# Kernel tuning notes

Hardware: AMD Instinct MI355X
Metric: run time of the kernel (lower is better)

The kernel has to match this reference:

```python
import jax, jax.numpy as jnp
import numpy as np

H = 256   # input_size
P = 256   # state_size
BATCH, L = 8, 4096
DT_MIN, DT_MAX = 1e-3, 1e-1
LN_EPS = 1e-5


def _hippo_params():
    # HiPPO-N matrix (num_blocks=1), eigendecomposition in numpy (float64 then cast)
    idx = np.arange(P, dtype=np.float64)
    s = np.sqrt(idx + 0.5)
    A = -np.outer(s, s)
    A = np.tril(A) - np.triu(A, 1)
    np.fill_diagonal(A, -0.5)
    ev, V = np.linalg.eig(A)
    order = np.argsort(ev.real)
    ev, V = ev[order], V[:, order]
    return ev, V


def setup_inputs() -> dict:
    key = jax.random.key(0)
    k_u, = jax.random.split(key, 1)
    ev, V = _hippo_params()
    rng = np.random.default_rng(0)
    log_lambda_real = np.log(-np.clip(ev.real, None, -1e-4)).astype(np.float32)
    lambda_imag = ev.imag.astype(np.float32)
    V_inv = np.linalg.inv(V)
    B_init = rng.standard_normal((P, H)) / np.sqrt(P)
    B_tilde = V_inv @ B_init.astype(np.complex128)
    C_init = rng.standard_normal((H, P)) / np.sqrt(P)
    C_tilde = C_init.astype(np.complex128) @ V
    log_delta = (rng.random(P) * (np.log(DT_MAX) - np.log(DT_MIN)) + np.log(DT_MIN)).astype(np.float32)
    return {
        "u": jax.random.normal(k_u, (BATCH, L, H), dtype=jnp.float32),
        "log_lambda_real": jnp.asarray(log_lambda_real),
        "lambda_imag": jnp.asarray(lambda_imag),
        "B_tilde_real": jnp.asarray(B_tilde.real, dtype=jnp.float32),
        "B_tilde_imag": jnp.asarray(B_tilde.imag, dtype=jnp.float32),
        "C_tilde_real": jnp.asarray(C_tilde.real, dtype=jnp.float32),
        "C_tilde_imag": jnp.asarray(C_tilde.imag, dtype=jnp.float32),
        "log_delta": jnp.asarray(log_delta),
        "gamma": jnp.ones((H,), dtype=jnp.float32),
        "beta": jnp.zeros((H,), dtype=jnp.float32),
    }


def _layernorm(x, gamma, beta):
    mu = jnp.mean(x, axis=-1, keepdims=True)
    var = jnp.mean(jnp.square(x - mu), axis=-1, keepdims=True)
    return (x - mu) * jax.lax.rsqrt(var + LN_EPS) * gamma + beta


def _ssm(h, log_lambda_real, lambda_imag, B_tilde_real, B_tilde_imag,
         C_tilde_real, C_tilde_imag, log_delta):
    # Continuous-time diagonal SSM params
    lam = -jnp.exp(log_lambda_real) + 1j * lambda_imag            # (P,) complex
    B_tilde = B_tilde_real + 1j * B_tilde_imag                     # (P,H)
    C_tilde = C_tilde_real + 1j * C_tilde_imag                     # (H,P)
    delta = jnp.exp(log_delta)                                     # (P,)
    # ZOH discretization (eq. 6 of the S5 paper)
    lambda_bar = jnp.exp(lam * delta)                              # (P,)
    B_bar = ((lambda_bar - 1.0) / lam)[:, None] * B_tilde          # (P,H)
    # Bu_k = B_bar @ u_k  ->  (B,L,P) complex
    Bu = jnp.einsum('blh,ph->blp', h.astype(jnp.complex64), B_bar.astype(jnp.complex64))
    # Parallel associative scan for x_k = lambda_bar * x_{k-1} + Bu_k
    a = jnp.broadcast_to(lambda_bar.astype(jnp.complex64), Bu.shape)
    def combine(c1, c2):
        a1, b1 = c1
        a2, b2 = c2
        return a1 * a2, a2 * b1 + b2
    _, xs = jax.lax.associative_scan(combine, (a, Bu), axis=1)     # (B,L,P)
    # Project back to real output: y = Re(C_tilde @ x)
    y = jnp.einsum('blp,hp->blh', xs, C_tilde.astype(jnp.complex64)).real
    return y


def reference(u, log_lambda_real, lambda_imag, B_tilde_real, B_tilde_imag,
              C_tilde_real, C_tilde_imag, log_delta, gamma, beta):
    # S5Block: pre-LayerNorm -> S5 SSM -> GELU -> residual
    h = _layernorm(u, gamma, beta)
    y = _ssm(h, log_lambda_real, lambda_imag, B_tilde_real, B_tilde_imag,
             C_tilde_real, C_tilde_imag, log_delta)
    return u + jax.nn.gelu(y)
```

## Files before the change

### kernel.cpp

```cpp
#include <hip/hip_runtime.h>
#include <math.h>

#define HDIM 256
#define PDIM 256
#define BATCH 8
#define LSEQ 4096
#define MTOT (BATCH * LSEQ)
#define NCHUNK 128
#define CHLEN 32

typedef __attribute__((ext_vector_type(8))) short bf16x8;
typedef __attribute__((ext_vector_type(4))) float f32x4;

__device__ __forceinline__ unsigned short f2bf(float f) {
    union { float f; unsigned int u; } v; v.f = f;
    unsigned int r = v.u + 0x7FFFu + ((v.u >> 16) & 1u);
    return (unsigned short)(r >> 16);
}
__device__ __forceinline__ float bf2f(unsigned int lo16) {
    union { unsigned int u; float f; } v; v.u = lo16 << 16;
    return v.f;
}

__global__ void params_k(const float* __restrict__ llr, const float* __restrict__ lim,
                         const float* __restrict__ ldl, float* __restrict__ par) {
    int p = threadIdx.x;
    float er = expf(llr[p]);
    float im = lim[p];
    float d  = expf(ldl[p]);
    float zr = -er * d, zi = im * d;
    float ea = expf(zr);
    float ar = ea * cosf(zi), ai = ea * sinf(zi);
    float dr = -er, di = im;
    float den = dr * dr + di * di;
    float nr = ar - 1.0f, ni = ai;
    float cr = (nr * dr + ni * di) / den;
    float ci = (ni * dr - nr * di) / den;
    float eC = expf((float)CHLEN * zr);
    float sC, cC;
    sincosf((float)CHLEN * zi, &sC, &cC);
    par[2 * p]           = ar;
    par[2 * p + 1]       = ai;
    par[512 + 2 * p]     = cr;
    par[512 + 2 * p + 1] = ci;
    par[1024 + 2 * p]     = eC * cC;
    par[1024 + 2 * p + 1] = eC * sC;
}

__global__ void w1_k(const float* __restrict__ Br, const float* __restrict__ Bi,
                     const float* __restrict__ par, unsigned short* __restrict__ W1t) {
    int p = blockIdx.x, h = threadIdx.x;
    float cr = par[512 + 2 * p], ci = par[512 + 2 * p + 1];
    float br = Br[p * HDIM + h], bi = Bi[p * HDIM + h];
    W1t[(2 * p) * HDIM + h]     = f2bf(cr * br - ci * bi);
    W1t[(2 * p + 1) * HDIM + h] = f2bf(cr * bi + ci * br);
}

__global__ void w2_k(const float* __restrict__ Cr, const float* __restrict__ Ci,
                     unsigned short* __restrict__ W2t) {
    int p = blockIdx.x, h = threadIdx.x;
    W2t[h * (2 * PDIM) + 2 * p]     = f2bf(Cr[h * PDIM + p]);
    W2t[h * (2 * PDIM) + 2 * p + 1] = f2bf(-Ci[h * PDIM + p]);
}

__global__ void ln_k(const float* __restrict__ u, unsigned short* __restrict__ hbf,
                     const float* __restrict__ gamma, const float* __restrict__ beta) {
    __shared__ float gS[HDIM], bS[HDIM];
    int t = threadIdx.x;
    gS[t] = gamma[t]; bS[t] = beta[t];
    int lane = t & 63, wv = t >> 6;
    int row = blockIdx.x * 4 + wv;
    float4 v = *(const float4*)(u + (size_t)row * HDIM + lane * 4);
    float s  = v.x + v.y + v.z + v.w;
    float sq = v.x * v.x + v.y * v.y + v.z * v.z + v.w * v.w;
    #pragma unroll
    for (int o = 1; o < 64; o <<= 1) { s += __shfl_xor(s, o); sq += __shfl_xor(sq, o); }
    float mu = s * (1.0f / HDIM);
    float rs = rsqrtf(sq * (1.0f / HDIM) - mu * mu + 1e-5f);
    __syncthreads();
    int c = lane * 4;
    ushort4 o;
    o.x = f2bf((v.x - mu) * rs * gS[c + 0] + bS[c + 0]);
    o.y = f2bf((v.y - mu) * rs * gS[c + 1] + bS[c + 1]);
    o.z = f2bf((v.z - mu) * rs * gS[c + 2] + bS[c + 2]);
    o.w = f2bf((v.w - mu) * rs * gS[c + 3] + bS[c + 3]);
    *(ushort4*)(hbf + (size_t)row * HDIM + c) = o;
}

#define LDK 40

template <int MODE>
__launch_bounds__(256, 2)
__global__ void mfma_gemm_k(const unsigned short* __restrict__ A,
                            const unsigned short* __restrict__ B,
                            void* __restrict__ outv,
                            const float* __restrict__ u,
                            int N, int K) {
    __shared__ unsigned short As[128 * LDK];
    __shared__ unsigned short Bs[128 * LDK];
    const int t = threadIdx.x;
    const int bn = blockIdx.x, bm = blockIdx.y;
    const int lane = t & 63;
    const int wm = ((t >> 6) & 1) * 64;
    const int wn = ((t >> 6) >> 1) * 64;
    const int srow = t >> 1, skoff = (t & 1) * 16;
    const unsigned short* Ap = A + (size_t)(bm * 128 + srow) * K + skoff;
    const unsigned short* Bp = B + (size_t)(bn * 128 + srow) * K + skoff;
    unsigned short* AsW = &As[srow * LDK + skoff];
    unsigned short* BsW = &Bs[srow * LDK + skoff];
    const int mrow = lane & 15;
    const int kq = (lane >> 4) * 8;

    f32x4 acc[4][4] = {};

    for (int k0 = 0; k0 < K; k0 += 32) {
        uint4 a0 = *(const uint4*)(Ap + k0);
        uint4 a1 = *(const uint4*)(Ap + k0 + 8);
        uint4 b0 = *(const uint4*)(Bp + k0);
        uint4 b1 = *(const uint4*)(Bp + k0 + 8);
        __syncthreads();
        *(uint4*)AsW       = a0;
        *(uint4*)(AsW + 8) = a1;
        *(uint4*)BsW       = b0;
        *(uint4*)(BsW + 8) = b1;
        __syncthreads();
        bf16x8 fa[4], fb[4];
        #pragma unroll
        for (int i = 0; i < 4; i++) {
            fa[i] = *(const bf16x8*)&As[(wm + i * 16 + mrow) * LDK + kq];
            fb[i] = *(const bf16x8*)&Bs[(wn + i * 16 + mrow) * LDK + kq];
        }
        #pragma unroll
        for (int i = 0; i < 4; i++)
            #pragma unroll
            for (int j = 0; j < 4; j++)
                acc[i][j] = __builtin_amdgcn_mfma_f32_16x16x32_bf16(fa[i], fb[j], acc[i][j], 0, 0, 0);
    }

    const int r0 = (lane >> 4) * 4;
    const int c0 = lane & 15;
    #pragma unroll
    for (int i = 0; i < 4; i++) {
        #pragma unroll
        for (int r = 0; r < 4; r++) {
            const size_t rowoff = (size_t)(bm * 128 + wm + i * 16 + r0 + r) * N;
            #pragma unroll
            for (int j = 0; j < 4; j++) {
                const int col_g = bn * 128 + wn + j * 16 + c0;
                float y = acc[i][j][r];
                if (MODE == 0) {
                    ((unsigned short*)outv)[rowoff + col_g] = f2bf(y);
                } else {
                    float z = 0.7978845608f * fmaf(0.044715f * y * y, y, y);
                    float e = __expf(2.0f * z);
                    float th = 1.0f - 2.0f / (e + 1.0f);
                    float g = 0.5f * y * (1.0f + th);
                    ((float*)outv)[rowoff + col_g] = u[rowoff + col_g] + g;
                }
            }
        }
    }
}

__global__ void scan_reduce_k(const unsigned short* __restrict__ Bu,
                              const float* __restrict__ par, float* __restrict__ last) {
    int p = threadIdx.x, c = blockIdx.x, b = blockIdx.y;
    float ar = par[2 * p], ai = par[2 * p + 1];
    float xr = 0.0f, xi = 0.0f;
    const unsigned int* q = (const unsigned int*)(Bu + ((size_t)b * LSEQ + (size_t)c * CHLEN) * 512) + p;
    #pragma unroll 8
    for (int j = 0; j < CHLEN; j++) {
        unsigned int v = q[j * 256];
        float vr = bf2f(v & 0xFFFFu), vi = bf2f(v >> 16);
        float nr = fmaf(ar, xr, fmaf(-ai, xi, vr));
        float ni = fmaf(ar, xi, fmaf(ai, xr, vi));
        xr = nr; xi = ni;
    }
    *(float2*)(last + ((size_t)b * NCHUNK + c) * 512 + 2 * p) = make_float2(xr, xi);
}

__global__ void scan_carry_k(const float* __restrict__ last, float* __restrict__ prefix,
                             const float* __restrict__ par) {
    int p = threadIdx.x, b = blockIdx.x;
    float Ar = par[1024 + 2 * p], Ai = par[1024 + 2 * p + 1];
    float Pr = 0.0f, Pi = 0.0f;
    for (int c = 0; c < NCHUNK; c++) {
        size_t idx = ((size_t)b * NCHUNK + c) * 512 + 2 * p;
        *(float2*)(prefix + idx) = make_float2(Pr, Pi);
        float2 l = *(const float2*)(last + idx);
        float nr = fmaf(Ar, Pr, fmaf(-Ai, Pi, l.x));
        float ni = fmaf(Ar, Pi, fmaf(Ai, Pr, l.y));
        Pr = nr; Pi = ni;
    }
}

__global__ void scan_apply_k(unsigned short* __restrict__ Bu, const float* __restrict__ par,
                             const float* __restrict__ prefix) {
    int p = threadIdx.x, c = blockIdx.x, b = blockIdx.y;
    float ar = par[2 * p], ai = par[2 * p + 1];
    float2 P = *(const float2*)(prefix + ((size_t)b * NCHUNK + c) * 512 + 2 * p);
    float xr = P.x, xi = P.y;
    unsigned int* q = (unsigned int*)(Bu + ((size_t)b * LSEQ + (size_t)c * CHLEN) * 512) + p;
    #pragma unroll 8
    for (int j = 0; j < CHLEN; j++) {
        unsigned int v = q[j * 256];
        float vr = bf2f(v & 0xFFFFu), vi = bf2f(v >> 16);
        float nr = fmaf(ar, xr, fmaf(-ai, xi, vr));
        float ni = fmaf(ar, xi, fmaf(ai, xr, vi));
        xr = nr; xi = ni;
        q[j * 256] = (unsigned int)f2bf(xr) | ((unsigned int)f2bf(xi) << 16);
    }
}

extern "C" void kernel_launch(void* const* d_in, const int* in_sizes, int n_in,
                              void* d_out, int out_size, void* d_ws, size_t ws_size,
                              hipStream_t stream) {
    const float* u   = (const float*)d_in[0];
    const float* llr = (const float*)d_in[1];
    const float* lim = (const float*)d_in[2];
    const float* Br  = (const float*)d_in[3];
    const float* Bi  = (const float*)d_in[4];
    const float* Cr  = (const float*)d_in[5];
    const float* Ci  = (const float*)d_in[6];
    const float* ldl = (const float*)d_in[7];
    const float* gam = (const float*)d_in[8];
    const float* bet = (const float*)d_in[9];
    float* out = (float*)d_out;

    float* ws     = (float*)d_ws;
    float* par    = ws;
    float* last   = ws + 2048;
    float* prefix = last + (size_t)BATCH * NCHUNK * 512;
    unsigned short* W1t = (unsigned short*)(prefix + (size_t)BATCH * NCHUNK * 512);
    unsigned short* W2t = W1t + 512 * HDIM;
    unsigned short* hbf = W2t + HDIM * 512;
    unsigned short* Bu  = hbf + (size_t)MTOT * HDIM;

    params_k<<<1, PDIM, 0, stream>>>(llr, lim, ldl, par);
    w1_k<<<PDIM, HDIM, 0, stream>>>(Br, Bi, par, W1t);
    w2_k<<<PDIM, HDIM, 0, stream>>>(Cr, Ci, W2t);
    ln_k<<<MTOT / 4, 256, 0, stream>>>(u, hbf, gam, bet);

    mfma_gemm_k<0><<<dim3(512 / 128, MTOT / 128), 256, 0, stream>>>(
        hbf, W1t, (void*)Bu, nullptr, 512, HDIM);

    scan_reduce_k<<<dim3(NCHUNK, BATCH), PDIM, 0, stream>>>(Bu, par, last);
    scan_carry_k<<<BATCH, PDIM, 0, stream>>>(last, prefix, par);
    scan_apply_k<<<dim3(NCHUNK, BATCH), PDIM, 0, stream>>>(Bu, par, prefix);

    mfma_gemm_k<1><<<dim3(HDIM / 128, MTOT / 128), 256, 0, stream>>>(
        Bu, W2t, (void*)out, u, HDIM, 512);
}
```

Baseline: 175.0 us.

## Fuse chunked scan into both GEMMs with precomputed lambda powers for carry fixup

The first GEMM now runs the intra-chunk scan in shared memory on its 128-row output tile and writes chunk-local states plus chunk tails. The second GEMM applies the inter-chunk carry on the fly using precomputed powers of lambda_bar as it loads A tiles. This removes the separate scan_reduce and scan_apply passes over the large Bu buffer, and chunk length grows to 128. The trade-off is a serial 128-step scan done by only 64 threads per block inside gemm1, extra fp32 loads of the power and prefix tables in gemm2, and removal of the LDS padding, which may cause bank conflicts.

```diff
diff --git a/kernel.cpp b/kernel.cpp
--- a/kernel.cpp
+++ b/kernel.cpp
@@ -6,8 +6,8 @@
 #define BATCH 8
 #define LSEQ 4096
 #define MTOT (BATCH * LSEQ)
-#define NCHUNK 128
-#define CHLEN 32
+#define CHLEN 128
+#define NCHUNK 32
 
 typedef __attribute__((ext_vector_type(8))) short bf16x8;
 typedef __attribute__((ext_vector_type(4))) float f32x4;
@@ -23,8 +23,34 @@
 }
 
 __global__ void params_k(const float* __restrict__ llr, const float* __restrict__ lim,
-                         const float* __restrict__ ldl, float* __restrict__ par) {
+                         const float* __restrict__ ldl, float* __restrict__ par,
+                         float* __restrict__ apw) {
     int p = threadIdx.x;
+    float er = expf(llr[p]);
+    float im = lim[p];
+    float d  = expf(ldl[p]);
+    float zr = -er * d, zi = im * d;
+    float ea = expf(zr);
+    float ar = ea * cosf(zi), ai = ea * sinf(zi);
+    par[2 * p]     = ar;
+    par[2 * p + 1] = ai;
+    float pr = ar, pi = ai;
+    apw[2 * p] = pr; apw[2 * p + 1] = pi;
+    for (int j = 1; j < CHLEN; j++) {
+        float nr = pr * ar - pi * ai;
+        float ni = pr * ai + pi * ar;
+        pr = nr; pi = ni;
+        apw[j * 512 + 2 * p]     = pr;
+        apw[j * 512 + 2 * p + 1] = pi;
+    }
+}
+
+__global__ void w12_k(const float* __restrict__ Br, const float* __restrict__ Bi,
+                      const float* __restrict__ Cr, const float* __restrict__ Ci,
+                      const float* __restrict__ llr, const float* __restrict__ lim,
+                      const float* __restrict__ ldl,
+                      unsigned short* __restrict__ W1t, unsigned short* __restrict__ W2t) {
+    int p = blockIdx.x, h = threadIdx.x;
     float er = expf(llr[p]);
     float im = lim[p];
     float d  = expf(ldl[p]);
@@ -36,31 +62,11 @@
     float nr = ar - 1.0f, ni = ai;
     float cr = (nr * dr + ni * di) / den;
     float ci = (ni * dr - nr * di) / den;
-    float eC = expf((float)CHLEN * zr);
-    float sC, cC;
-    sincosf((float)CHLEN * zi, &sC, &cC);
-    par[2 * p]           = ar;
-    par[2 * p + 1]       = ai;
-    par[512 + 2 * p]     = cr;
-    par[512 + 2 * p + 1] = ci;
-    par[1024 + 2 * p]     = eC * cC;
-    par[1024 + 2 * p + 1] = eC * sC;
-}
-
-__global__ void w1_k(const float* __restrict__ Br, const float* __restrict__ Bi,
-                     const float* __restrict__ par, unsigned short* __restrict__ W1t) {
-    int p = blockIdx.x, h = threadIdx.x;
-    float cr = par[512 + 2 * p], ci = par[512 + 2 * p + 1];
     float br = Br[p * HDIM + h], bi = Bi[p * HDIM + h];
     W1t[(2 * p) * HDIM + h]     = f2bf(cr * br - ci * bi);
     W1t[(2 * p + 1) * HDIM + h] = f2bf(cr * bi + ci * br);
-}
-
-__global__ void w2_k(const float* __restrict__ Cr, const float* __restrict__ Ci,
-                     unsigned short* __restrict__ W2t) {
-    int p = blockIdx.x, h = threadIdx.x;
-    W2t[h * (2 * PDIM) + 2 * p]     = f2bf(Cr[h * PDIM + p]);
-    W2t[h * (2 * PDIM) + 2 * p + 1] = f2bf(-Ci[h * PDIM + p]);
+    W2t[h * 512 + 2 * p]     = f2bf(Cr[h * PDIM + p]);
+    W2t[h * 512 + 2 * p + 1] = f2bf(-Ci[h * PDIM + p]);
 }
 
 __global__ void ln_k(const float* __restrict__ u, unsigned short* __restrict__ hbf,
@@ -87,48 +93,43 @@
     *(ushort4*)(hbf + (size_t)row * HDIM + c) = o;
 }
 
-#define LDK 40
-
-template <int MODE>
 __launch_bounds__(256, 2)
-__global__ void mfma_gemm_k(const unsigned short* __restrict__ A,
-                            const unsigned short* __restrict__ B,
-                            void* __restrict__ outv,
-                            const float* __restrict__ u,
-                            int N, int K) {
-    __shared__ unsigned short As[128 * LDK];
-    __shared__ unsigned short Bs[128 * LDK];
+__global__ void gemm1_k(const unsigned short* __restrict__ A, const unsigned short* __restrict__ B,
+                        unsigned short* __restrict__ Bu, float* __restrict__ last,
+                        const float* __restrict__ par, const float* __restrict__ apw) {
+    __shared__ union {
+        struct { unsigned short A[128 * 32]; unsigned short B[128 * 32]; } st;
+        unsigned short C[128 * 128];
+    } sm;
+
     const int t = threadIdx.x;
     const int bn = blockIdx.x, bm = blockIdx.y;
     const int lane = t & 63;
     const int wm = ((t >> 6) & 1) * 64;
     const int wn = ((t >> 6) >> 1) * 64;
     const int srow = t >> 1, skoff = (t & 1) * 16;
-    const unsigned short* Ap = A + (size_t)(bm * 128 + srow) * K + skoff;
-    const unsigned short* Bp = B + (size_t)(bn * 128 + srow) * K + skoff;
-    unsigned short* AsW = &As[srow * LDK + skoff];
-    unsigned short* BsW = &Bs[srow * LDK + skoff];
-    const int mrow = lane & 15;
-    const int kq = (lane >> 4) * 8;
+    const unsigned short* Ap = A + (size_t)(bm * 128 + srow) * 256 + skoff;
+    const unsigned short* Bp = B + (size_t)(bn * 128 + srow) * 256 + skoff;
+    const int mrow = lane & 15, kq = (lane >> 4) * 8;
 
     f32x4 acc[4][4] = {};
 
-    for (int k0 = 0; k0 < K; k0 += 32) {
+    for (int k0 = 0; k0 < 256; k0 += 32) {
         uint4 a0 = *(const uint4*)(Ap + k0);
         uint4 a1 = *(const uint4*)(Ap + k0 + 8);
         uint4 b0 = *(const uint4*)(Bp + k0);
         uint4 b1 = *(const uint4*)(Bp + k0 + 8);
         __syncthreads();
-        *(uint4*)AsW       = a0;
-        *(uint4*)(AsW + 8) = a1;
-        *(uint4*)BsW       = b0;
-        *(uint4*)(BsW + 8) = b1;
+        *(uint4*)&sm.st.A[srow * 32 + skoff]     = a0;
+        *(uint4*)&sm.st.A[srow * 32 + skoff + 8] = a1;
+        *(uint4*)&sm.st.B[srow * 32 + skoff]     = b0;
+        *(uint4*)&sm.st.B[srow * 32 + skoff + 8] = b1;
         __syncthreads();
         bf16x8 fa[4], fb[4];
         #pragma unroll
         for (int i = 0; i < 4; i++) {
-            fa[i] = *(const bf16x8*)&As[(wm + i * 16 + mrow) * LDK + kq];
-            fb[i] = *(const bf16x8*)&Bs[(wn + i * 16 + mrow) * LDK + kq];
+            fa[i] = *(const bf16x8*)&sm.st.A[(wm + i * 16 + mrow) * 32 + kq];
+            fb[i] = *(const bf16x8*)&sm.st.B[(wn + i * 16 + mrow) * 32 + kq];
         }
         #pragma unroll
         for (int i = 0; i < 4; i++)
@@ -137,55 +138,52 @@
                 acc[i][j] = __builtin_amdgcn_mfma_f32_16x16x32_bf16(fa[i], fb[j], acc[i][j], 0, 0, 0);
     }
 
-    const int r0 = (lane >> 4) * 4;
-    const int c0 = lane & 15;
+    __syncthreads();
+    const int r0 = (lane >> 4) * 4, c0 = lane & 15;
     #pragma unroll
-    for (int i = 0; i < 4; i++) {
-        #pragma unroll
-        for (int r = 0; r < 4; r++) {
-            const size_t rowoff = (size_t)(bm * 128 + wm + i * 16 + r0 + r) * N;
+    for (int i = 0; i < 4; i++)
+        #pragma unroll
+        for (int j = 0; j < 4; j++)
             #pragma unroll
-            for (int j = 0; j < 4; j++) {
-                const int col_g = bn * 128 + wn + j * 16 + c0;
-                float y = acc[i][j][r];
-                if (MODE == 0) {
-                    ((unsigned short*)outv)[rowoff + col_g] = f2bf(y);
-                } else {
-                    float z = 0.7978845608f * fmaf(0.044715f * y * y, y, y);
-                    float e = __expf(2.0f * z);
-                    float th = 1.0f - 2.0f / (e + 1.0f);
-                    float g = 0.5f * y * (1.0f + th);
-                    ((float*)outv)[rowoff + col_g] = u[rowoff + col_g] + g;
-                }
-            }
-        }
-    }
-}
-
-__global__ void scan_reduce_k(const unsigned short* __restrict__ Bu,
-                              const float* __restrict__ par, float* __restrict__ last) {
-    int p = threadIdx.x, c = blockIdx.x, b = blockIdx.y;
-    float ar = par[2 * p], ai = par[2 * p + 1];
-    float xr = 0.0f, xi = 0.0f;
-    const unsigned int* q = (const unsigned int*)(Bu + ((size_t)b * LSEQ + (size_t)c * CHLEN) * 512) + p;
-    #pragma unroll 8
-    for (int j = 0; j < CHLEN; j++) {
-        unsigned int v = q[j * 256];
-        float vr = bf2f(v & 0xFFFFu), vi = bf2f(v >> 16);
-        float nr = fmaf(ar, xr, fmaf(-ai, xi, vr));
-        float ni = fmaf(ar, xi, fmaf(ai, xr, vi));
-        xr = nr; xi = ni;
-    }
-    *(float2*)(last + ((size_t)b * NCHUNK + c) * 512 + 2 * p) = make_float2(xr, xi);
-}
-
-__global__ void scan_carry_k(const float* __restrict__ last, float* __restrict__ prefix,
-                             const float* __restrict__ par) {
+            for (int r = 0; r < 4; r++)
+                sm.C[(wm + i * 16 + r0 + r) * 128 + wn + j * 16 + c0] = f2bf(acc[i][j][r]);
+    __syncthreads();
+
+    if (t < 64) {
+        int pg = bn * 64 + t;
+        float ar = par[2 * pg], ai = par[2 * pg + 1];
+        float xr = 0.0f, xi = 0.0f;
+        unsigned int* Cw = (unsigned int*)sm.C;
+        #pragma unroll 8
+        for (int s = 0; s < CHLEN; s++) {
+            unsigned int v = Cw[s * 64 + t];
+            float vr = bf2f(v & 0xFFFFu), vi = bf2f(v >> 16);
+            float nr = fmaf(ar, xr, fmaf(-ai, xi, vr));
+            float ni = fmaf(ar, xi, fmaf(ai, xr, vi));
+            xr = nr; xi = ni;
+            Cw[s * 64 + t] = (unsigned int)f2bf(xr) | ((unsigned int)f2bf(xi) << 16);
+        }
+        *(float2*)(last + (size_t)(bm * 256 + pg) * 2) = make_float2(xr, xi);
+    }
+    __syncthreads();
+
+    {
+        int row = t >> 1, ch = (t & 1) * 64;
+        unsigned short* dst = Bu + (size_t)(bm * 128 + row) * 512 + bn * 128 + ch;
+        const unsigned short* src = &sm.C[row * 128 + ch];
+        #pragma unroll
+        for (int q = 0; q < 8; q++)
+            *(uint4*)(dst + q * 8) = *(const uint4*)(src + q * 8);
+    }
+}
+
+__global__ void carry_k(const float* __restrict__ last, float* __restrict__ prefix,
+                        const float* __restrict__ apw) {
     int p = threadIdx.x, b = blockIdx.x;
-    float Ar = par[1024 + 2 * p], Ai = par[1024 + 2 * p + 1];
+    float Ar = apw[127 * 512 + 2 * p], Ai = apw[127 * 512 + 2 * p + 1];
     float Pr = 0.0f, Pi = 0.0f;
     for (int c = 0; c < NCHUNK; c++) {
-        size_t idx = ((size_t)b * NCHUNK + c) * 512 + 2 * p;
+        size_t idx = (size_t)((b * NCHUNK + c) * 256 + p) * 2;
         *(float2*)(prefix + idx) = make_float2(Pr, Pi);
         float2 l = *(const float2*)(last + idx);
         float nr = fmaf(Ar, Pr, fmaf(-Ai, Pi, l.x));
@@ -194,21 +192,84 @@
     }
 }
 
-__global__ void scan_apply_k(unsigned short* __restrict__ Bu, const float* __restrict__ par,
-                             const float* __restrict__ prefix) {
-    int p = threadIdx.x, c = blockIdx.x, b = blockIdx.y;
-    float ar = par[2 * p], ai = par[2 * p + 1];
-    float2 P = *(const float2*)(prefix + ((size_t)b * NCHUNK + c) * 512 + 2 * p);
-    float xr = P.x, xi = P.y;
-    unsigned int* q = (unsigned int*)(Bu + ((size_t)b * LSEQ + (size_t)c * CHLEN) * 512) + p;
-    #pragma unroll 8
-    for (int j = 0; j < CHLEN; j++) {
-        unsigned int v = q[j * 256];
-        float vr = bf2f(v & 0xFFFFu), vi = bf2f(v >> 16);
-        float nr = fmaf(ar, xr, fmaf(-ai, xi, vr));
-        float ni = fmaf(ar, xi, fmaf(ai, xr, vi));
-        xr = nr; xi = ni;
-        q[j * 256] = (unsigned int)f2bf(xr) | ((unsigned int)f2bf(xi) << 16);
+__launch_bounds__(256, 2)
+__global__ void gemm2_k(const unsigned short* __restrict__ Bu, const unsigned short* __restrict__ B,
+                        float* __restrict__ out, const float* __restrict__ u,
+                        const float* __restrict__ apw, const float* __restrict__ prefix) {
+    __shared__ struct { unsigned short A[128 * 32]; unsigned short B[128 * 32]; } st;
+    const int t = threadIdx.x;
+    const int bn = blockIdx.x, bm = blockIdx.y;
+    const int lane = t & 63;
+    const int wm = ((t >> 6) & 1) * 64;
+    const int wn = ((t >> 6) >> 1) * 64;
+    const int srow = t >> 1, skoff = (t & 1) * 16;
+    const unsigned short* Ap = Bu + (size_t)(bm * 128 + srow) * 512 + skoff;
+    const unsigned short* Bp = B + (size_t)(bn * 128 + srow) * 512 + skoff;
+    const float* fw = apw + srow * 512 + skoff;
+    const float* pw = prefix + (size_t)bm * 512 + skoff;
+    const int mrow = lane & 15, kq = (lane >> 4) * 8;
+
+    f32x4 acc[4][4] = {};
+
+    for (int k0 = 0; k0 < 512; k0 += 32) {
+        uint4 q0 = *(const uint4*)(Ap + k0);
+        uint4 q1 = *(const uint4*)(Ap + k0 + 8);
+        uint4 b0 = *(const uint4*)(Bp + k0);
+        uint4 b1 = *(const uint4*)(Bp + k0 + 8);
+        float4 f0 = *(const float4*)(fw + k0),     f1 = *(const float4*)(fw + k0 + 4);
+        float4 f2 = *(const float4*)(fw + k0 + 8), f3 = *(const float4*)(fw + k0 + 12);
+        float4 g0 = *(const float4*)(pw + k0),     g1 = *(const float4*)(pw + k0 + 4);
+        float4 g2 = *(const float4*)(pw + k0 + 8), g3 = *(const float4*)(pw + k0 + 12);
+        __syncthreads();
+        unsigned int qa[8] = {q0.x, q0.y, q0.z, q0.w, q1.x, q1.y, q1.z, q1.w};
+        float fv[16], pv[16];
+        *(float4*)&fv[0] = f0;  *(float4*)&fv[4] = f1;  *(float4*)&fv[8] = f2;  *(float4*)&fv[12] = f3;
+        *(float4*)&pv[0] = g0;  *(float4*)&pv[4] = g1;  *(float4*)&pv[8] = g2;  *(float4*)&pv[12] = g3;
+        unsigned int xo[8];
+        #pragma unroll
+        for (int e = 0; e < 8; e++) {
+            float vr = bf2f(qa[e] & 0xFFFFu), vi = bf2f(qa[e] >> 16);
+            float fr = fv[2 * e], fi = fv[2 * e + 1];
+            float Pr = pv[2 * e], Pi = pv[2 * e + 1];
+            float xr = fmaf(fr, Pr, fmaf(-fi, Pi, vr));
+            float xi = fmaf(fr, Pi, fmaf(fi, Pr, vi));
+            xo[e] = (unsigned int)f2bf(xr) | ((unsigned int)f2bf(xi) << 16);
+        }
+        *(uint4*)&st.A[srow * 32 + skoff]     = make_uint4(xo[0], xo[1], xo[2], xo[3]);
+        *(uint4*)&st.A[srow * 32 + skoff + 8] = make_uint4(xo[4], xo[5], xo[6], xo[7]);
+        *(uint4*)&st.B[srow * 32 + skoff]     = b0;
+        *(uint4*)&st.B[srow * 32 + skoff + 8] = b1;
+        __syncthreads();
+        bf16x8 fa[4], fb[4];
+        #pragma unroll
+        for (int i = 0; i < 4; i++) {
+            fa[i] = *(const bf16x8*)&st.A[(wm + i * 16 + mrow) * 32 + kq];
+            fb[i] = *(const bf16x8*)&st.B[(wn + i * 16 + mrow) * 32 + kq];
+        }
+        #pragma unroll
+        for (int i = 0; i < 4; i++)
+            #pragma unroll
+            for (int j = 0; j < 4; j++)
+                acc[i][j] = __builtin_amdgcn_mfma_f32_16x16x32_bf16(fa[i], fb[j], acc[i][j], 0, 0, 0);
+    }
+
+    const int r0 = (lane >> 4) * 4, c0 = lane & 15;
+    #pragma unroll
+    for (int i = 0; i < 4; i++) {
+        #pragma unroll
+        for (int r = 0; r < 4; r++) {
+            const size_t rowoff = (size_t)(bm * 128 + wm + i * 16 + r0 + r) * 256;
+            #pragma unroll
+            for (int j = 0; j < 4; j++) {
+                const int col = bn * 128 + wn + j * 16 + c0;
+                float y = acc[i][j][r];
+                float z = 0.7978845608f * fmaf(0.044715f * y * y, y, y);
+                float e = __expf(2.0f * z);
+                float th = 1.0f - 2.0f / (e + 1.0f);
+                float g = 0.5f * y * (1.0f + th);
+                out[rowoff + col] = u[rowoff + col] + g;
+            }
+        }
     }
 }
 
@@ -229,25 +290,21 @@
 
     float* ws     = (float*)d_ws;
     float* par    = ws;
-    float* last   = ws + 2048;
-    float* prefix = last + (size_t)BATCH * NCHUNK * 512;
-    unsigned short* W1t = (unsigned short*)(prefix + (size_t)BATCH * NCHUNK * 512);
+    float* apw    = ws + 1024;
+    float* last   = apw + 128 * 512;
+    float* prefix = last + 256 * 256 * 2;
+    unsigned short* W1t = (unsigned short*)(prefix + 256 * 256 * 2);
     unsigned short* W2t = W1t + 512 * HDIM;
     unsigned short* hbf = W2t + HDIM * 512;
     unsigned short* Bu  = hbf + (size_t)MTOT * HDIM;
 
-    params_k<<<1, PDIM, 0, stream>>>(llr, lim, ldl, par);
-    w1_k<<<PDIM, HDIM, 0, stream>>>(Br, Bi, par, W1t);
-    w2_k<<<PDIM, HDIM, 0, stream>>>(Cr, Ci, W2t);
+    params_k<<<1, PDIM, 0, stream>>>(llr, lim, ldl, par, apw);
+    w12_k<<<PDIM, HDIM, 0, stream>>>(Br, Bi, Cr, Ci, llr, lim, ldl, W1t, W2t);
     ln_k<<<MTOT / 4, 256, 0, stream>>>(u, hbf, gam, bet);
 
-    mfma_gemm_k<0><<<dim3(512 / 128, MTOT / 128), 256, 0, stream>>>(
-        hbf, W1t, (void*)Bu, nullptr, 512, HDIM);
-
-    scan_reduce_k<<<dim3(NCHUNK, BATCH), PDIM, 0, stream>>>(Bu, par, last);
-    scan_carry_k<<<BATCH, PDIM, 0, stream>>>(last, prefix, par);
-    scan_apply_k<<<dim3(NCHUNK, BATCH), PDIM, 0, stream>>>(Bu, par, prefix);
-
-    mfma_gemm_k<1><<<dim3(HDIM / 128, MTOT / 128), 256, 0, stream>>>(
-        Bu, W2t, (void*)out, u, HDIM, 512);
-}
+    gemm1_k<<<dim3(4, MTOT / 128), 256, 0, stream>>>(hbf, W1t, Bu, last, par, apw);
+
+    carry_k<<<BATCH, PDIM, 0, stream>>>(last, prefix, apw);
+
+    gemm2_k<<<dim3(2, MTOT / 128), 256, 0, stream>>>(Bu, W2t, out, u, apw, prefix);
+}
```

Measured after the change: 184.6 us. 1.05x slower.
